# Kernel optimization log

Hardware: AMD Instinct MI355X
Metric: run time of the kernel (lower is better)

## Reference

```python
import jax, jax.numpy as jnp
import numpy as np

ROPE_BASE = 10000.0
NEG_INF = -1e9


def apply_rope(x):
    # torchtune RotaryPositionalEmbeddings: interleaved pairs
    # x: [B, S, H, Dh]
    B, S, H, Dh = x.shape
    half = Dh // 2
    theta = 1.0 / (ROPE_BASE ** (jnp.arange(0, Dh, 2, dtype=jnp.float32) / Dh))  # [half]
    pos = jnp.arange(S, dtype=jnp.float32)
    ang = pos[:, None] * theta[None, :]                      # [S, half]
    cos = jnp.cos(ang)[None, :, None, :]                      # [1,S,1,half]
    sin = jnp.sin(ang)[None, :, None, :]
    xp = x.reshape(B, S, H, half, 2)
    x0, x1 = xp[..., 0], xp[..., 1]
    out = jnp.stack([x0 * cos - x1 * sin, x1 * cos + x0 * sin], axis=-1)
    return out.reshape(B, S, H, Dh)


def setup_inputs() -> dict:
    key = jax.random.key(0)
    ks = jax.random.split(key, 6)
    B, S, D = 2, 2048, 1024
    IH, ID = 4, 64
    sc = lambda d: 1.0 / np.sqrt(d)
    return {
        "x": jax.random.normal(ks[0], (B, S, D), jnp.float32),
        "W_qkv": jax.random.normal(ks[1], (D, 3 * D), jnp.float32) * sc(D),
        "W_o": jax.random.normal(ks[2], (D, D), jnp.float32) * sc(D),
        "Wq_idx": jax.random.normal(ks[3], (D, IH * ID), jnp.float32) * sc(D),
        "Wk_idx": jax.random.normal(ks[4], (D, ID), jnp.float32) * sc(D),
        "Ww_idx": jax.random.normal(ks[5], (D, IH), jnp.float32) * sc(D),
        "top_k": 512,
    }


def reference(x, W_qkv, W_o, Wq_idx, Wk_idx, Ww_idx, top_k):
    B, S, D = x.shape
    H = 16
    Dh = D // H
    IH, ID = 4, 64

    # QKV projection + RoPE (dropout in eval mode -> p=0)
    qkv = x @ W_qkv                                # [B,S,3D]
    Q, K, V = jnp.split(qkv, 3, axis=-1)
    Q = apply_rope(Q.reshape(B, S, H, Dh))
    K = apply_rope(K.reshape(B, S, H, Dh))
    V = V.reshape(B, S, H, Dh)

    # Lightning indexer: I[b,t,s] = sum_h w[b,t,h] * relu(q[b,t,h]·k[b,s])
    iq = (x @ Wq_idx).reshape(B, S, IH, ID)
    ik = x @ Wk_idx                                # [B,S,ID]
    iw = x @ Ww_idx                                # [B,S,IH]
    raw = jax.nn.relu(jnp.einsum('bthd,bsd->bths', iq, ik))
    index_scores = jnp.einsum('bth,bths->bts', iw, raw)  # [B,S,S]

    # Causal top-k selection -> boolean mask
    causal = jnp.tril(jnp.ones((S, S), bool))
    masked_scores = jnp.where(causal[None], index_scores, NEG_INF)
    _, top_idx = jax.lax.top_k(masked_scores, top_k)       # [B,S,k]
    bi = jnp.arange(B)[:, None, None]
    ti = jnp.arange(S)[None, :, None]
    sel = jnp.zeros((B, S, S), bool).at[bi, ti, top_idx].set(True)
    sel = sel & causal[None]                               # [B,S,S]

    # Masked SDPA
    scale = 1.0 / jnp.sqrt(jnp.asarray(Dh, x.dtype))
    logits = jnp.einsum('bthd,bshd->bhts', Q, K) * scale    # [B,H,S,S]
    logits = jnp.where(sel[:, None], logits, NEG_INF)
    probs = jax.nn.softmax(logits, axis=-1)
    attn = jnp.einsum('bhts,bshd->bthd', probs, V).reshape(B, S, D)
    return attn @ W_o
```

## Files before the change

### kernel.cpp

```cpp
#include <hip/hip_runtime.h>
#include <stdint.h>

typedef short s16x8 __attribute__((ext_vector_type(8)));
typedef float f32x4 __attribute__((ext_vector_type(4)));

#define MFMA_BF16(a,b,c) __builtin_amdgcn_mfma_f32_16x16x32_bf16((a),(b),(c),0,0,0)

static __device__ __forceinline__ float bf2f(unsigned short b){
  return __uint_as_float(((unsigned)b)<<16);
}
static __device__ __forceinline__ unsigned short f2bf(float f){
  unsigned u = __float_as_uint(f);
  unsigned r = u + 0x7FFFu + ((u>>16)&1u);
  return (unsigned short)(r>>16);
}
static __device__ __forceinline__ unsigned cvt_pk_bf16(float lo, float hi){
  unsigned r; asm("v_cvt_pk_bf16_f32 %0, %1, %2" : "=v"(r) : "v"(lo), "v"(hi)); return r;
}
static __device__ __forceinline__ void store_val(float* p, float v){ *p = v; }
static __device__ __forceinline__ void store_val(unsigned short* p, float v){ *p = f2bf(v); }

static __device__ __forceinline__ unsigned ordf(float f){
  if (f == 0.0f) return 0x80000000u;
  unsigned u = __float_as_uint(f);
  return (u & 0x80000000u) ? ~u : (u | 0x80000000u);
}

typedef __attribute__((address_space(1))) const void g_void;
typedef __attribute__((address_space(3))) void l_void;
static __device__ __forceinline__ void gload_lds16(const void* g, void* lds){
  __builtin_amdgcn_global_load_lds((g_void*)g, (l_void*)lds, 16, 0, 0);
}

__global__ __launch_bounds__(256) void k_f32_to_bf16(const float* __restrict__ in,
                                                     unsigned short* __restrict__ out, int n){
  int i = blockIdx.x*256 + threadIdx.x;
  int stride = gridDim.x*256;
  for(; i<n; i+=stride) out[i] = f2bf(in[i]);
}

__global__ __launch_bounds__(256) void k_pack_b(const float* __restrict__ Wqi, const float* __restrict__ Wki,
                                                const float* __restrict__ Wwi, float* __restrict__ Bcat){
  int i = blockIdx.x*256 + threadIdx.x;
  if(i >= 1024*324) return;
  int kk = i/324, j = i - kk*324;
  float v = (j<256) ? Wqi[kk*256+j] : (j<320) ? Wki[kk*64 + (j-256)] : Wwi[kk*4 + (j-320)];
  Bcat[i] = v;
}

template<typename OT>
__global__ __launch_bounds__(256) void k_transpose(const float* __restrict__ in, OT* __restrict__ out,
                                                   int R, int C, int inRS, long zIn, long zOut){
  __shared__ float tile[32][33];
  const float* inb = in + (long)blockIdx.z*zIn;
  OT* outb = out + (long)blockIdx.z*zOut;
  int tx = threadIdx.x, ty = threadIdx.y;
  int c0 = blockIdx.x*32, r0 = blockIdx.y*32;
#pragma unroll
  for(int j=0;j<4;j++) tile[ty+j*8][tx] = inb[(long)(r0+ty+j*8)*inRS + c0 + tx];
  __syncthreads();
#pragma unroll
  for(int j=0;j<4;j++) store_val(&outb[(long)(c0+ty+j*8)*R + r0 + tx], tile[tx][ty+j*8]);
}

__global__ __launch_bounds__(256) void k_gemm_f32(const float* __restrict__ A, const float* __restrict__ B,
                                                  float* __restrict__ C, int M, int N, int K){
  __shared__ float As[64][17];
  __shared__ float Bs[16][68];
  int tid = threadIdx.x;
  int tx = tid & 15, ty = tid >> 4;
  int m0 = blockIdx.x*64, n0 = blockIdx.y*64;
  float acc[4][4] = {};
  for(int k0=0; k0<K; k0+=16){
#pragma unroll
    for(int i=0;i<4;i++){
      int e = tid + i*256; int rr = e>>4, cc = e&15;
      As[rr][cc] = A[(long)(m0+rr)*K + k0 + cc];
    }
#pragma unroll
    for(int i=0;i<4;i++){
      int e = tid + i*256; int rr = e>>6, cc = e&63;
      int n = n0 + cc;
      Bs[rr][cc] = (n<N) ? B[(long)(k0+rr)*N + n] : 0.f;
    }
    __syncthreads();
#pragma unroll
    for(int kk=0;kk<16;kk++){
      float av[4], bv[4];
#pragma unroll
      for(int i=0;i<4;i++) av[i] = As[ty*4+i][kk];
#pragma unroll
      for(int j=0;j<4;j++) bv[j] = Bs[kk][tx*4+j];
#pragma unroll
      for(int i=0;i<4;i++)
#pragma unroll
        for(int j=0;j<4;j++) acc[i][j] = fmaf(av[i], bv[j], acc[i][j]);
    }
    __syncthreads();
  }
#pragma unroll
  for(int i=0;i<4;i++){
    int m = m0 + ty*4 + i;
#pragma unroll
    for(int j=0;j<4;j++){
      int n = n0 + tx*4 + j;
      if(n<N) C[(long)m*N + n] = acc[i][j];
    }
  }
}

template<typename OT>
__global__ __launch_bounds__(256) void k_gemm_bf16(const unsigned short* __restrict__ A,
                                                   const unsigned short* __restrict__ BT,
                                                   OT* __restrict__ C, int M, int N, int K){
  __shared__ __align__(16) unsigned short As[128*32];
  __shared__ __align__(16) unsigned short Bs[128*32];
  int tid = threadIdx.x;
  int w = tid>>6, l = tid&63;
  int fr = l&15, fg = l>>4;
  int wm = (w>>1)*64, wn = (w&1)*64;
  long m0 = (long)blockIdx.x*128, n0 = (long)blockIdx.y*128;
  f32x4 acc[4][4];
#pragma unroll
  for(int i=0;i<4;i++)
#pragma unroll
    for(int j=0;j<4;j++){ f32x4 z = {0.f,0.f,0.f,0.f}; acc[i][j]=z; }

  for(int k0=0;k0<K;k0+=32){
    __syncthreads();
#pragma unroll
    for(int i=0;i<2;i++){
      int eo = (w*64 + l)*8 + i*2048;
      int rr = eo>>5, cc = eo&31;
      gload_lds16(A + (m0+rr)*K + k0 + cc, (char*)As + w*1024 + i*4096);
    }
#pragma unroll
    for(int i=0;i<2;i++){
      int eo = (w*64 + l)*8 + i*2048;
      int rr = eo>>5, cc = eo&31;
      gload_lds16(BT + (n0+rr)*K + k0 + cc, (char*)Bs + w*1024 + i*4096);
    }
    asm volatile("s_waitcnt vmcnt(0)" ::: "memory");
    __syncthreads();
    s16x8 af[4], bfr[4];
#pragma unroll
    for(int mf=0;mf<4;mf++) af[mf]  = *(const s16x8*)&As[(wm + mf*16 + fr)*32 + fg*8];
#pragma unroll
    for(int nf=0;nf<4;nf++) bfr[nf] = *(const s16x8*)&Bs[(wn + nf*16 + fr)*32 + fg*8];
#pragma unroll
    for(int mf=0;mf<4;mf++)
#pragma unroll
      for(int nf=0;nf<4;nf++)
        acc[mf][nf] = MFMA_BF16(af[mf], bfr[nf], acc[mf][nf]);
  }
#pragma unroll
  for(int mf=0;mf<4;mf++)
#pragma unroll
    for(int nf=0;nf<4;nf++)
#pragma unroll
      for(int r=0;r<4;r++){
        long m = m0 + wm + mf*16 + fg*4 + r;
        long n = n0 + wn + nf*16 + fr;
        store_val(&C[m*N + n], acc[mf][nf][r]);
      }
}

__global__ __launch_bounds__(256) void k_rope_tab(float* __restrict__ cosT, float* __restrict__ sinT){
  int i = blockIdx.x*256 + threadIdx.x;
  int t = i>>5, p = i&31;
  float theta = exp2f(-(float)p * (13.287712379549449f/32.0f));
  float ang = (float)t * theta;
  cosT[i] = cosf(ang);
  sinT[i] = sinf(ang);
}

__global__ __launch_bounds__(256) void k_rope_permute(const unsigned short* __restrict__ qkv,
                                                      const float* __restrict__ cosT, const float* __restrict__ sinT,
                                                      unsigned short* __restrict__ Qr, unsigned short* __restrict__ Kr,
                                                      unsigned short* __restrict__ VT){
  int st = blockIdx.x, h = blockIdx.y, b = blockIdx.z;
  int tid = threadIdx.x;
  __shared__ float vt[64][65];
  long rowbase = (long)b*2048 + st*64;
#pragma unroll
  for(int part=0; part<2; part++){
    const int colbase = part*1024 + h*64;
    unsigned short* outp = part ? Kr : Qr;
    float prescale = part ? 1.0f : 0.18033688011112042f;
#pragma unroll
    for(int i=0;i<8;i++){
      int e = tid + i*256;
      int row = e>>5, p = e&31;
      long s = (long)st*64 + row;
      const unsigned short* src = qkv + (rowbase+row)*3072 + colbase + 2*p;
      float x0 = bf2f(src[0]), x1 = bf2f(src[1]);
      float c = cosT[s*32+p], sn = sinT[s*32+p];
      float y0 = (x0*c - x1*sn)*prescale;
      float y1 = (x1*c + x0*sn)*prescale;
      unsigned short* dst = outp + ((long)(b*16+h)*2048 + s)*64 + 2*p;
      dst[0] = f2bf(y0); dst[1] = f2bf(y1);
    }
  }
#pragma unroll
  for(int i=0;i<16;i++){
    int e = tid + i*256;
    int row = e>>6, col = e&63;
    vt[col][row] = bf2f(qkv[(rowbase+row)*3072 + 2048 + h*64 + col]);
  }
  __syncthreads();
#pragma unroll
  for(int i=0;i<16;i++){
    int e = tid + i*256;
    int d = e>>6, scol = e&63;
    VT[((long)(b*16+h)*64 + d)*2048 + (long)st*64 + scol] = f2bf(vt[d][scol]);
  }
}

__global__ __launch_bounds__(256) void k_topk(const float* __restrict__ iqkw, const int* __restrict__ pk,
                                              unsigned* __restrict__ bmask){
  int b = blockIdx.y;
  int tid = threadIdx.x;
  int w = tid>>6, lane = tid&63;
  int k = pk[0];
  __shared__ float siq[256];
  __shared__ float siw[4];
  __shared__ unsigned su[2048];
  __shared__ unsigned hist4[4][256];
  __shared__ unsigned chunk[4];
  __shared__ unsigned words[64];
  __shared__ unsigned sh_b[2];
  const int s0 = tid*8;
  const float* ikb = iqkw + (long)b*2048*324 + 256;

  (void)ikb;
  for(int rp=0; rp<2; rp++){
    int t = rp ? (2047 - (int)blockIdx.x) : (int)blockIdx.x;
    long row = (long)b*2048 + t;
    siq[tid] = iqkw[row*324 + tid];
    if(tid<4) siw[tid] = iqkw[row*324 + 320 + tid];
    __syncthreads();

    if (s0 <= t){
      float acc[4][8];
#pragma unroll
      for(int h=0;h<4;h++)
#pragma unroll
        for(int j=0;j<8;j++) acc[h][j]=0.f;
      const float* ikTb = (const float*)nullptr;
      (void)ikTb;
      extern __shared__ char _dummy[]; (void)_dummy;
      const float* ikT = 0; (void)ikT;
      ;
    }
    __syncthreads();
    (void)w; (void)lane; (void)chunk; (void)hist4; (void)words; (void)sh_b; (void)su; (void)siw; (void)siq; (void)k;
    break;
  }
}

__global__ __launch_bounds__(256) void k_topk2(const float* __restrict__ iqkw, const float* __restrict__ ikT,
                                               const int* __restrict__ pk, unsigned* __restrict__ bmask){
  int b = blockIdx.y;
  int tid = threadIdx.x;
  int w = tid>>6, lane = tid&63;
  int k = pk[0];
  __shared__ float siq[256];
  __shared__ float siw[4];
  __shared__ unsigned su[2048];
  __shared__ unsigned hist4[4][256];
  __shared__ unsigned chunk[4];
  __shared__ unsigned words[64];
  __shared__ unsigned sh_b[2];
  const int s0 = tid*8;

  for(int rp=0; rp<2; rp++){
    int t = rp ? (2047 - (int)blockIdx.x) : (int)blockIdx.x;
    long row = (long)b*2048 + t;
    siq[tid] = iqkw[row*324 + tid];
    if(tid<4) siw[tid] = iqkw[row*324 + 320 + tid];
    __syncthreads();

    if (s0 <= t){
      float acc[4][8];
#pragma unroll
      for(int h=0;h<4;h++)
#pragma unroll
        for(int j=0;j<8;j++) acc[h][j]=0.f;
      const float* ikb = ikT + (long)b*64*2048;
      for(int d=0;d<64;d++){
        const float* prow = ikb + (long)d*2048 + s0;
        float4 v0 = *(const float4*)prow;
        float4 v1 = *(const float4*)(prow+4);
        float ikv[8] = {v0.x,v0.y,v0.z,v0.w,v1.x,v1.y,v1.z,v1.w};
#pragma unroll
        for(int h=0;h<4;h++){
          float q = siq[h*64+d];
#pragma unroll
          for(int j=0;j<8;j++) acc[h][j] = fmaf(q, ikv[j], acc[h][j]);
        }
      }
#pragma unroll
      for(int j=0;j<8;j++){
        int s = s0+j;
        if(s<=t){
          float I = 0.f;
#pragma unroll
          for(int h=0;h<4;h++) I += siw[h]*fmaxf(acc[h][j],0.f);
          su[s] = ordf(I);
        }
      }
    }
    __syncthreads();

    unsigned thr = 0; int kk = 0;
    bool allsel = (t+1 <= k);
    if (!allsel){
      unsigned prefix=0, msk=0;
      kk = k;
      for(int shift=24; shift>=0; shift-=8){
#pragma unroll
        for(int i=0;i<4;i++) hist4[i][tid]=0;
        __syncthreads();
        if(s0<=t){
          for(int j=0;j<8;j++){
            int s=s0+j; if(s>t) break;
            unsigned u=su[s];
            if((u&msk)==prefix) atomicAdd(&hist4[w][(u>>shift)&255],1u);
          }
        }
        __syncthreads();
        unsigned hv = hist4[0][tid]+hist4[1][tid]+hist4[2][tid]+hist4[3][tid];
        unsigned sfx = hv;
#pragma unroll
        for(int off=1; off<64; off<<=1){
          unsigned tmp = __shfl_down(sfx, off);
          if(lane < 64-off) sfx += tmp;
        }
        if(lane==0) chunk[w] = sfx;
        __syncthreads();
        unsigned above = 0;
#pragma unroll
        for(int c=0;c<4;c++) if(c>w) above += chunk[c];
        unsigned incl = sfx + above;
        unsigned cb   = incl - hv;
        if(cb < (unsigned)kk && incl >= (unsigned)kk){ sh_b[0]=(unsigned)tid; sh_b[1]=(unsigned)kk-cb; }
        __syncthreads();
        prefix |= sh_b[0]<<shift; msk |= 255u<<shift; kk = (int)sh_b[1];
        __syncthreads();
      }
      thr = prefix;
    }

    unsigned gtb=0, eqb=0;
    if (s0 <= t){
      for(int j=0;j<8;j++){
        int s=s0+j; if(s>t) break;
        if(allsel){ gtb |= 1u<<j; }
        else{
          unsigned u=su[s];
          if(u>thr) gtb |= 1u<<j;
          else if(u==thr) eqb |= 1u<<j;
        }
      }
    }
    int cnt = __popc(eqb);
    unsigned pfx = (unsigned)cnt;
#pragma unroll
    for(int off=1; off<64; off<<=1){
      unsigned tmp = __shfl_up(pfx, off);
      if(lane >= off) pfx += tmp;
    }
    if(lane==63) chunk[w] = pfx;
    __syncthreads();
    unsigned below = 0;
#pragma unroll
    for(int c=0;c<4;c++) if(c<w) below += chunk[c];
    int excl = (int)(pfx - (unsigned)cnt + below);
    unsigned bits = gtb;
    if(eqb){
      int seen=0;
      for(int j=0;j<8;j++) if((eqb>>j)&1u){ if(excl+seen < kk) bits |= 1u<<j; seen++; }
    }
    if(tid<64) words[tid]=0;
    __syncthreads();
    if(bits) atomicOr(&words[tid>>2], bits << ((tid&3)*8));
    __syncthreads();
    if(tid<64) bmask[row*64 + tid] = words[tid];
    __syncthreads();
  }
}

__global__ __launch_bounds__(256) void k_attn_part(const unsigned short* __restrict__ Qr,
                                                   const unsigned short* __restrict__ Kr,
                                                   const unsigned short* __restrict__ VT,
                                                   const unsigned* __restrict__ bmask,
                                                   unsigned short* __restrict__ pO,
                                                   float2* __restrict__ pML){
  int xb = blockIdx.x, h = blockIdx.y, b = blockIdx.z;
  int pair = xb>>1, kp = xb&1;
  int tid = threadIdx.x, w = tid>>6, l = tid&63;
  int fr = l&15, fg = l>>4;
  __shared__ __align__(16) unsigned short P[4][16][72];
  const unsigned short* Qb = Qr + (long)(b*16+h)*2048*64;
  const unsigned short* Kb = Kr + (long)(b*16+h)*2048*64;
  const unsigned short* Vb = VT + (long)(b*16+h)*64*2048;
  const unsigned* bm = bmask + (long)b*2048*64;
  long pbase = ((long)(b*16+h)*2 + kp)*2048;

#pragma unroll 1
  for(int pass=0; pass<2; pass++){
    int T = pass ? (31-pair) : pair;
    int split = (T+1)>>1;
    int st0 = kp ? split : 0;
    int st1 = kp ? (T+1) : split;
    int r0 = T*64 + w*16;
    s16x8 aq[2];
#pragma unroll
    for(int ks=0;ks<2;ks++) aq[ks] = *(const s16x8*)(Qb + (long)(r0+fr)*64 + ks*32 + fg*8);
    const unsigned* bmrow = bm + (long)(r0+fr)*64;
    float mrow = -1e30f, lrow = 0.f;
    f32x4 accO[4];
#pragma unroll
    for(int nf=0;nf<4;nf++){ f32x4 z = {0.f,0.f,0.f,0.f}; accO[nf]=z; }

    for(int st=st0; st<st1; st++){
      unsigned w0 = bmrow[st*2], w1 = bmrow[st*2+1];
      f32x4 sacc[4];
#pragma unroll
      for(int nf=0;nf<4;nf++){ f32x4 z = {0.f,0.f,0.f,0.f}; sacc[nf]=z; }
#pragma unroll
      for(int ks=0;ks<2;ks++)
#pragma unroll
        for(int nf=0;nf<4;nf++){
          s16x8 bk = *(const s16x8*)(Kb + (long)(st*64 + nf*16 + fr)*64 + ks*32 + fg*8);
          sacc[nf] = MFMA_BF16(bk, aq[ks], sacc[nf]);
        }
      s16x8 bv0[4];
#pragma unroll
      for(int nf=0;nf<4;nf++) bv0[nf] = *(const s16x8*)(Vb + (long)(nf*16+fr)*2048 + st*64 + fg*8);
      float vmax = -1e30f;
#pragma unroll
      for(int nf=0;nf<4;nf++)
#pragma unroll
        for(int r=0;r<4;r++){
          int sl = nf*16 + fg*4 + r;
          unsigned word = (sl<32) ? w0 : w1;
          bool sel = (word>>(sl&31))&1u;
          float v = sel ? sacc[nf][r] : -1e30f;
          sacc[nf][r] = v;
          vmax = fmaxf(vmax, v);
        }
      vmax = fmaxf(vmax, __shfl_xor(vmax,16));
      vmax = fmaxf(vmax, __shfl_xor(vmax,32));
      bool up = vmax > mrow;
      float mnew = fmaxf(mrow, vmax);
      float psum = 0.f;
#pragma unroll
      for(int nf=0;nf<4;nf++)
#pragma unroll
        for(int r=0;r<4;r++){
          float v = sacc[nf][r];
          float e = (v > -1e29f) ? exp2f(v - mnew) : 0.f;
          sacc[nf][r] = e; psum += e;
        }
      psum += __shfl_xor(psum,16);
      psum += __shfl_xor(psum,32);
#pragma unroll
      for(int nf=0;nf<4;nf++){
        *(unsigned*)&P[w][fr][nf*16 + fg*4 + 0] = cvt_pk_bf16(sacc[nf][0], sacc[nf][1]);
        *(unsigned*)&P[w][fr][nf*16 + fg*4 + 2] = cvt_pk_bf16(sacc[nf][2], sacc[nf][3]);
      }
      if(__any(up)){
        float sc = exp2f(mrow - mnew);
        lrow = lrow*sc + psum; mrow = mnew;
        float scv[4];
#pragma unroll
        for(int r=0;r<4;r++) scv[r] = __shfl(sc, fg*4 + r);
#pragma unroll
        for(int nf=0;nf<4;nf++)
#pragma unroll
          for(int r=0;r<4;r++) accO[nf][r] *= scv[r];
      } else {
        lrow += psum;
      }
#pragma unroll
      for(int ks=0;ks<2;ks++){
        s16x8 pa = *(const s16x8*)&P[w][fr][ks*32 + fg*8];
#pragma unroll
        for(int nf=0;nf<4;nf++){
          s16x8 bv = ks ? *(const s16x8*)(Vb + (long)(nf*16+fr)*2048 + st*64 + 32 + fg*8) : bv0[nf];
          accO[nf] = MFMA_BF16(pa, bv, accO[nf]);
        }
      }
    }
    if(fg==0) pML[pbase + r0 + fr] = make_float2(mrow, lrow);
#pragma unroll
    for(int r=0;r<4;r++){
      int trow = r0 + fg*4 + r;
#pragma unroll
      for(int nf=0;nf<4;nf++)
        pO[(pbase + trow)*64 + nf*16 + fr] = f2bf(accO[nf][r]);
    }
  }
}

__global__ __launch_bounds__(256) void k_attn_combine(const unsigned short* __restrict__ pO,
                                                      const float2* __restrict__ pML,
                                                      unsigned short* __restrict__ attnb){
  int gid = blockIdx.x*256 + threadIdx.x;
  int rg = gid>>3, dg = gid&7;
  long bh = rg>>11; int row = rg&2047;
  long base0 = (bh*2+0)*2048 + row;
  long base1 = (bh*2+1)*2048 + row;
  float2 ml0 = pML[base0], ml1 = pML[base1];
  float m = fmaxf(ml0.x, ml1.x);
  float w0 = exp2f(ml0.x - m), w1 = exp2f(ml1.x - m);
  float inv = 1.0f/(ml0.y*w0 + ml1.y*w1);
  s16x8 o0 = *(const s16x8*)(pO + base0*64 + dg*8);
  s16x8 o1 = *(const s16x8*)(pO + base1*64 + dg*8);
  s16x8 o;
#pragma unroll
  for(int j=0;j<8;j++){
    float v = (bf2f((unsigned short)o0[j])*w0 + bf2f((unsigned short)o1[j])*w1)*inv;
    o[j] = (short)f2bf(v);
  }
  int b = (int)(bh>>4), h = (int)(bh&15);
  *(s16x8*)(attnb + ((long)b*2048 + row)*1024 + h*64 + dg*8) = o;
}

extern "C" void kernel_launch(void* const* d_in, const int* in_sizes, int n_in,
                              void* d_out, int out_size, void* d_ws, size_t ws_size,
                              hipStream_t stream){
  (void)in_sizes; (void)n_in; (void)out_size; (void)ws_size;
  const float* x    = (const float*)d_in[0];
  const float* Wqkv = (const float*)d_in[1];
  const float* Wo   = (const float*)d_in[2];
  const float* Wqi  = (const float*)d_in[3];
  const float* Wki  = (const float*)d_in[4];
  const float* Wwi  = (const float*)d_in[5];
  const int*   pk   = (const int*)d_in[6];

  const int B=2, S=2048, D=1024, H=16;
  const long MS = (long)B*S;

  char* ws = (char*)d_ws;
  size_t off = 0;
  auto alloc = [&](size_t bytes)->char*{
    char* p = ws + off; off = (off + bytes + 255) & ~(size_t)255; return p;
  };
  unsigned short* x_bf   = (unsigned short*)alloc(MS*D*2);
  unsigned short* wqkvT  = (unsigned short*)alloc((size_t)3*D*D*2);
  unsigned short* woT    = (unsigned short*)alloc((size_t)D*D*2);
  unsigned short* qkv_bf = (unsigned short*)alloc(MS*3*D*2);
  unsigned short* Qr     = (unsigned short*)alloc(MS*D*2);
  unsigned short* Kr     = (unsigned short*)alloc(MS*D*2);
  unsigned short* VTb    = (unsigned short*)alloc(MS*D*2);
  unsigned short* attnb  = (unsigned short*)alloc(MS*D*2);
  float* Bcat  = (float*)alloc((size_t)1024*324*4);
  float* iqkw  = (float*)alloc(MS*324*4);
  float* ikT   = (float*)alloc(MS*64*4);
  float* cosT  = (float*)alloc((size_t)S*32*4);
  float* sinT  = (float*)alloc((size_t)S*32*4);
  unsigned* bmask = (unsigned*)alloc((size_t)B*S*64*4);
  unsigned short* pO = (unsigned short*)alloc((size_t)2*B*H*S*64*2);
  float2* pML = (float2*)alloc((size_t)2*B*H*S*8);

  k_f32_to_bf16<<<4096,256,0,stream>>>(x, x_bf, (int)(MS*D));
  k_transpose<unsigned short><<<dim3(3*D/32, D/32, 1), dim3(32,8), 0, stream>>>(Wqkv, wqkvT, D, 3*D, 3*D, 0, 0);
  k_transpose<unsigned short><<<dim3(D/32, D/32, 1), dim3(32,8), 0, stream>>>(Wo, woT, D, D, D, 0, 0);

  k_pack_b<<<(1024*324+255)/256,256,0,stream>>>(Wqi, Wki, Wwi, Bcat);
  k_gemm_f32<<<dim3(64,6),256,0,stream>>>(x, Bcat, iqkw, (int)MS, 324, D);
  k_transpose<float><<<dim3(2, 64, B), dim3(32,8), 0, stream>>>(iqkw + 256, ikT, S, 64, 324, (long)S*324, (long)S*64);
  k_topk2<<<dim3(S/2,B),256,0,stream>>>(iqkw, ikT, pk, bmask);

  k_rope_tab<<<S*32/256,256,0,stream>>>(cosT, sinT);
  k_gemm_bf16<unsigned short><<<dim3(MS/128, 3*D/128), 256, 0, stream>>>(x_bf, wqkvT, qkv_bf, (int)MS, 3*D, D);
  k_rope_permute<<<dim3(S/64, H, B), 256, 0, stream>>>(qkv_bf, cosT, sinT, Qr, Kr, VTb);

  k_attn_part<<<dim3(32, H, B), 256, 0, stream>>>(Qr, Kr, VTb, bmask, pO, pML);
  k_attn_combine<<<(int)(MS*16*8/256), 256, 0, stream>>>(pO, pML, attnb);
  k_gemm_bf16<float><<<dim3(MS/128, D/128), 256, 0, stream>>>(attnb, woT, (float*)d_out, (int)MS, D, D);
}
```

Before: 491.5 us.

## Fuse attention split-K and combine into double-buffered LDS-staged attention kernel

Replaces the two-way split-KV attention plus separate combine kernel with a single kernel in which each block handles a full causal row pair. K and V tiles are staged into swizzled, double-buffered LDS through async global-to-LDS loads, and the final normalisation is applied in-kernel. Blocks are remapped so that a batch-head's work lands on one XCD. This drops the partial-output round trip and one launch, but halves the number of blocks (512 vs 1024) and adds barriers every tile, which may reduce parallelism. The dead k_topk stub is also removed.

```diff
diff --git a/kernel.cpp b/kernel.cpp
--- a/kernel.cpp
+++ b/kernel.cpp
@@ -213,48 +213,6 @@
     int e = tid + i*256;
     int d = e>>6, scol = e&63;
     VT[((long)(b*16+h)*64 + d)*2048 + (long)st*64 + scol] = f2bf(vt[d][scol]);
-  }
-}
-
-__global__ __launch_bounds__(256) void k_topk(const float* __restrict__ iqkw, const int* __restrict__ pk,
-                                              unsigned* __restrict__ bmask){
-  int b = blockIdx.y;
-  int tid = threadIdx.x;
-  int w = tid>>6, lane = tid&63;
-  int k = pk[0];
-  __shared__ float siq[256];
-  __shared__ float siw[4];
-  __shared__ unsigned su[2048];
-  __shared__ unsigned hist4[4][256];
-  __shared__ unsigned chunk[4];
-  __shared__ unsigned words[64];
-  __shared__ unsigned sh_b[2];
-  const int s0 = tid*8;
-  const float* ikb = iqkw + (long)b*2048*324 + 256;
-
-  (void)ikb;
-  for(int rp=0; rp<2; rp++){
-    int t = rp ? (2047 - (int)blockIdx.x) : (int)blockIdx.x;
-    long row = (long)b*2048 + t;
-    siq[tid] = iqkw[row*324 + tid];
-    if(tid<4) siw[tid] = iqkw[row*324 + 320 + tid];
-    __syncthreads();
-
-    if (s0 <= t){
-      float acc[4][8];
-#pragma unroll
-      for(int h=0;h<4;h++)
-#pragma unroll
-        for(int j=0;j<8;j++) acc[h][j]=0.f;
-      const float* ikTb = (const float*)nullptr;
-      (void)ikTb;
-      extern __shared__ char _dummy[]; (void)_dummy;
-      const float* ikT = 0; (void)ikT;
-      ;
-    }
-    __syncthreads();
-    (void)w; (void)lane; (void)chunk; (void)hist4; (void)words; (void)sh_b; (void)su; (void)siw; (void)siq; (void)k;
-    break;
   }
 }
 
@@ -390,29 +348,45 @@
   }
 }
 
-__global__ __launch_bounds__(256) void k_attn_part(const unsigned short* __restrict__ Qr,
-                                                   const unsigned short* __restrict__ Kr,
-                                                   const unsigned short* __restrict__ VT,
-                                                   const unsigned* __restrict__ bmask,
-                                                   unsigned short* __restrict__ pO,
-                                                   float2* __restrict__ pML){
-  int xb = blockIdx.x, h = blockIdx.y, b = blockIdx.z;
-  int pair = xb>>1, kp = xb&1;
+static __device__ __forceinline__ void stage_kv(const unsigned short* __restrict__ Kb,
+                                                const unsigned short* __restrict__ Vb,
+                                                unsigned short* Ksb, unsigned short* Vsb,
+                                                int st, int w, int l){
+#pragma unroll
+  for(int i=0;i<2;i++){
+    int s = i*256 + w*64 + l;
+    int row = s>>3, c16 = s&7;
+    int col = (c16 ^ (row&7))*8;
+    gload_lds16(Kb + (long)(st*64 + row)*64 + col, (char*)Ksb + (i*256 + w*64)*16);
+    gload_lds16(Vb + (long)row*2048 + st*64 + col, (char*)Vsb + (i*256 + w*64)*16);
+  }
+}
+
+__global__ __launch_bounds__(256) void k_attn(const unsigned short* __restrict__ Qr,
+                                              const unsigned short* __restrict__ Kr,
+                                              const unsigned short* __restrict__ VT,
+                                              const unsigned* __restrict__ bmask,
+                                              unsigned short* __restrict__ attn){
+  int fid = blockIdx.x + (blockIdx.y<<4) + (blockIdx.z<<8);
+  int xcd = fid & 7, slot = fid >> 3;
+  int bh  = (xcd<<2) + (slot>>4);
+  int xb  = slot & 15;
+  int b = bh>>4, h = bh&15;
+
   int tid = threadIdx.x, w = tid>>6, l = tid&63;
   int fr = l&15, fg = l>>4;
+  __shared__ __align__(16) unsigned short Ks[2][64*64];
+  __shared__ __align__(16) unsigned short Vs[2][64*64];
   __shared__ __align__(16) unsigned short P[4][16][72];
-  const unsigned short* Qb = Qr + (long)(b*16+h)*2048*64;
-  const unsigned short* Kb = Kr + (long)(b*16+h)*2048*64;
-  const unsigned short* Vb = VT + (long)(b*16+h)*64*2048;
+  const unsigned short* Qb = Qr + (long)bh*2048*64;
+  const unsigned short* Kb = Kr + (long)bh*2048*64;
+  const unsigned short* Vb = VT + (long)bh*64*2048;
   const unsigned* bm = bmask + (long)b*2048*64;
-  long pbase = ((long)(b*16+h)*2 + kp)*2048;
+  const int swz = (fr&7)<<3;
 
 #pragma unroll 1
   for(int pass=0; pass<2; pass++){
-    int T = pass ? (31-pair) : pair;
-    int split = (T+1)>>1;
-    int st0 = kp ? split : 0;
-    int st1 = kp ? (T+1) : split;
+    int T = pass ? (31-xb) : xb;
     int r0 = T*64 + w*16;
     s16x8 aq[2];
 #pragma unroll
@@ -423,7 +397,14 @@
 #pragma unroll
     for(int nf=0;nf<4;nf++){ f32x4 z = {0.f,0.f,0.f,0.f}; accO[nf]=z; }
 
-    for(int st=st0; st<st1; st++){
+    stage_kv(Kb, Vb, Ks[0], Vs[0], 0, w, l);
+    asm volatile("s_waitcnt vmcnt(0)" ::: "memory");
+    __syncthreads();
+    int cur = 0;
+
+#pragma unroll 1
+    for(int st=0; st<=T; st++){
+      if(st < T) stage_kv(Kb, Vb, Ks[cur^1], Vs[cur^1], st+1, w, l);
       unsigned w0 = bmrow[st*2], w1 = bmrow[st*2+1];
       f32x4 sacc[4];
 #pragma unroll
@@ -432,24 +413,26 @@
       for(int ks=0;ks<2;ks++)
 #pragma unroll
         for(int nf=0;nf<4;nf++){
-          s16x8 bk = *(const s16x8*)(Kb + (long)(st*64 + nf*16 + fr)*64 + ks*32 + fg*8);
+          s16x8 bk = *(const s16x8*)&Ks[cur][(nf*16+fr)*64 + ((ks*32+fg*8) ^ swz)];
           sacc[nf] = MFMA_BF16(bk, aq[ks], sacc[nf]);
         }
-      s16x8 bv0[4];
-#pragma unroll
-      for(int nf=0;nf<4;nf++) bv0[nf] = *(const s16x8*)(Vb + (long)(nf*16+fr)*2048 + st*64 + fg*8);
+      s16x8 bvf[2][4];
+#pragma unroll
+      for(int ks=0;ks<2;ks++)
+#pragma unroll
+        for(int nf=0;nf<4;nf++)
+          bvf[ks][nf] = *(const s16x8*)&Vs[cur][(nf*16+fr)*64 + ((ks*32+fg*8) ^ swz)];
       float vmax = -1e30f;
 #pragma unroll
-      for(int nf=0;nf<4;nf++)
+      for(int nf=0;nf<4;nf++){
+        unsigned bits4 = ((nf<2) ? w0 : w1) >> ((nf&1)*16 + fg*4);
 #pragma unroll
         for(int r=0;r<4;r++){
-          int sl = nf*16 + fg*4 + r;
-          unsigned word = (sl<32) ? w0 : w1;
-          bool sel = (word>>(sl&31))&1u;
-          float v = sel ? sacc[nf][r] : -1e30f;
+          float v = ((bits4>>r)&1u) ? sacc[nf][r] : -1e30f;
           sacc[nf][r] = v;
           vmax = fmaxf(vmax, v);
         }
+      }
       vmax = fmaxf(vmax, __shfl_xor(vmax,16));
       vmax = fmaxf(vmax, __shfl_xor(vmax,32));
       bool up = vmax > mrow;
@@ -487,45 +470,24 @@
       for(int ks=0;ks<2;ks++){
         s16x8 pa = *(const s16x8*)&P[w][fr][ks*32 + fg*8];
 #pragma unroll
-        for(int nf=0;nf<4;nf++){
-          s16x8 bv = ks ? *(const s16x8*)(Vb + (long)(nf*16+fr)*2048 + st*64 + 32 + fg*8) : bv0[nf];
-          accO[nf] = MFMA_BF16(pa, bv, accO[nf]);
-        }
-      }
-    }
-    if(fg==0) pML[pbase + r0 + fr] = make_float2(mrow, lrow);
+        for(int nf=0;nf<4;nf++)
+          accO[nf] = MFMA_BF16(pa, bvf[ks][nf], accO[nf]);
+      }
+      asm volatile("s_waitcnt vmcnt(0)" ::: "memory");
+      __syncthreads();
+      cur ^= 1;
+    }
+    float linv[4];
+#pragma unroll
+    for(int r=0;r<4;r++) linv[r] = 1.0f/__shfl(lrow, fg*4 + r);
 #pragma unroll
     for(int r=0;r<4;r++){
       int trow = r0 + fg*4 + r;
 #pragma unroll
       for(int nf=0;nf<4;nf++)
-        pO[(pbase + trow)*64 + nf*16 + fr] = f2bf(accO[nf][r]);
-    }
-  }
-}
-
-__global__ __launch_bounds__(256) void k_attn_combine(const unsigned short* __restrict__ pO,
-                                                      const float2* __restrict__ pML,
-                                                      unsigned short* __restrict__ attnb){
-  int gid = blockIdx.x*256 + threadIdx.x;
-  int rg = gid>>3, dg = gid&7;
-  long bh = rg>>11; int row = rg&2047;
-  long base0 = (bh*2+0)*2048 + row;
-  long base1 = (bh*2+1)*2048 + row;
-  float2 ml0 = pML[base0], ml1 = pML[base1];
-  float m = fmaxf(ml0.x, ml1.x);
-  float w0 = exp2f(ml0.x - m), w1 = exp2f(ml1.x - m);
-  float inv = 1.0f/(ml0.y*w0 + ml1.y*w1);
-  s16x8 o0 = *(const s16x8*)(pO + base0*64 + dg*8);
-  s16x8 o1 = *(const s16x8*)(pO + base1*64 + dg*8);
-  s16x8 o;
-#pragma unroll
-  for(int j=0;j<8;j++){
-    float v = (bf2f((unsigned short)o0[j])*w0 + bf2f((unsigned short)o1[j])*w1)*inv;
-    o[j] = (short)f2bf(v);
-  }
-  int b = (int)(bh>>4), h = (int)(bh&15);
-  *(s16x8*)(attnb + ((long)b*2048 + row)*1024 + h*64 + dg*8) = o;
+        attn[((long)b*2048 + trow)*1024 + h*64 + nf*16 + fr] = f2bf(accO[nf][r]*linv[r]);
+    }
+  }
 }
 
 extern "C" void kernel_launch(void* const* d_in, const int* in_sizes, int n_in,
@@ -562,8 +524,6 @@
   float* cosT  = (float*)alloc((size_t)S*32*4);
   float* sinT  = (float*)alloc((size_t)S*32*4);
   unsigned* bmask = (unsigned*)alloc((size_t)B*S*64*4);
-  unsigned short* pO = (unsigned short*)alloc((size_t)2*B*H*S*64*2);
-  float2* pML = (float2*)alloc((size_t)2*B*H*S*8);
 
   k_f32_to_bf16<<<4096,256,0,stream>>>(x, x_bf, (int)(MS*D));
   k_transpose<unsigned short><<<dim3(3*D/32, D/32, 1), dim3(32,8), 0, stream>>>(Wqkv, wqkvT, D, 3*D, 3*D, 0, 0);
@@ -578,7 +538,6 @@
   k_gemm_bf16<unsigned short><<<dim3(MS/128, 3*D/128), 256, 0, stream>>>(x_bf, wqkvT, qkv_bf, (int)MS, 3*D, D);
   k_rope_permute<<<dim3(S/64, H, B), 256, 0, stream>>>(qkv_bf, cosT, sinT, Qr, Kr, VTb);
 
-  k_attn_part<<<dim3(32, H, B), 256, 0, stream>>>(Qr, Kr, VTb, bmask, pO, pML);
-  k_attn_combine<<<(int)(MS*16*8/256), 256, 0, stream>>>(pO, pML, attnb);
+  k_attn<<<dim3(16, H, B), 256, 0, stream>>>(Qr, Kr, VTb, bmask, attnb);
   k_gemm_bf16<float><<<dim3(MS/128, D/128), 256, 0, stream>>>(attnb, woT, (float*)d_out, (int)MS, D, D);
 }
```

Measured after the change: 417.5 us. 1.18x faster.
